# Performance work log

Measured on AMD Instinct MI355X. Metric: run time of the kernel, lower is better.

The kernel has to match this reference:

```python
import jax, jax.numpy as jnp
import numpy as np

N_HEADS = 16
D_EMBED = 1024
D_HEADS = D_EMBED // N_HEADS


def setup_inputs() -> dict:
    key = jax.random.key(0)
    k1, k2, k3, k4, k5 = jax.random.split(key, 5)
    B, S = 4, 2048
    x = jax.random.normal(k1, (B, S, D_EMBED), dtype=jnp.float32)
    s_in = 1.0 / np.sqrt(D_EMBED)
    in_proj_w = jax.random.normal(k2, (3 * D_EMBED, D_EMBED), dtype=jnp.float32) * s_in
    in_proj_b = jax.random.normal(k3, (3 * D_EMBED,), dtype=jnp.float32) * 0.01
    out_proj_w = jax.random.normal(k4, (D_EMBED, D_EMBED), dtype=jnp.float32) * s_in
    out_proj_b = jax.random.normal(k5, (D_EMBED,), dtype=jnp.float32) * 0.01
    return {"x": x, "in_proj_w": in_proj_w, "in_proj_b": in_proj_b,
            "out_proj_w": out_proj_w, "out_proj_b": out_proj_b}


def reference(x, in_proj_w, in_proj_b, out_proj_w, out_proj_b):
    B, S, D = x.shape
    # in_proj: Linear(d, 3d); torch chunks output as (k, q, v) in that order
    qkv = jnp.einsum('bsd,ed->bse', x, in_proj_w) + in_proj_b  # [B,S,3D]
    k, q, v = jnp.split(qkv, 3, axis=-1)
    # reshape to heads: [B, H, S, Dh]
    def to_heads(t):
        return t.reshape(B, S, N_HEADS, D_HEADS).transpose(0, 2, 1, 3)
    q, k, v = to_heads(q), to_heads(k), to_heads(v)
    scale = 1.0 / np.sqrt(D_HEADS)
    w = jnp.einsum('bhqd,bhkd->bhqk', q, k) * scale  # [B,H,S,S]
    w = jax.nn.softmax(w, axis=-1)
    score = jnp.einsum('bhqk,bhkd->bhqd', w, v)  # [B,H,S,Dh]
    score = score.transpose(0, 2, 1, 3).reshape(B, S, D)
    out = jnp.einsum('bsd,ed->bse', score, out_proj_w) + out_proj_b
    return out
```

## Files before the change

kernel.cpp:

```cpp
#include <hip/hip_runtime.h>

typedef __attribute__((ext_vector_type(8))) __bf16 bf16x8;
typedef __attribute__((ext_vector_type(4))) float  f32x4;
typedef __attribute__((ext_vector_type(4))) unsigned short us4;

#define QK_SCALE 0.180336880111112f

__device__ __forceinline__ unsigned short f2bf(float f) {
    unsigned u = __float_as_uint(f);
    u += 0x7fffu + ((u >> 16) & 1u);
    return (unsigned short)(u >> 16);
}

__device__ __forceinline__ unsigned cvt_pk_bf16(float lo, float hi) {
    unsigned r;
    asm("v_cvt_pk_bf16_f32 %0, %1, %2" : "=v"(r) : "v"(lo), "v"(hi));
    return r;
}

__device__ __forceinline__ void gload_lds16(const void* g, void* l) {
    __builtin_amdgcn_global_load_lds((const __attribute__((address_space(1))) void*)g,
                                     (__attribute__((address_space(3))) void*)l, 16, 0, 0);
}

__global__ __launch_bounds__(256) void f32_to_bf16_k(const float* __restrict__ in,
                                                     unsigned short* __restrict__ out, int n) {
    int i = (blockIdx.x * 256 + threadIdx.x) * 4;
    if (i + 3 < n) {
        float4 v = *(const float4*)(in + i);
        us4 o;
        o.x = f2bf(v.x); o.y = f2bf(v.y); o.z = f2bf(v.z); o.w = f2bf(v.w);
        *(us4*)(out + i) = o;
    }
}

__global__ __launch_bounds__(256) void cvt_w1_k(const float* __restrict__ in,
                                                unsigned short* __restrict__ out) {
    int i = (blockIdx.x * 256 + threadIdx.x) * 4;
    float4 v = *(const float4*)(in + i);
    const int row = i >> 10;
    const float s = (row >= 1024 && row < 2048) ? QK_SCALE : 1.0f;
    us4 o;
    o.x = f2bf(v.x * s); o.y = f2bf(v.y * s); o.z = f2bf(v.z * s); o.w = f2bf(v.w * s);
    *(us4*)(out + i) = o;
}

template <int OUTF, int QS>
__global__ __launch_bounds__(256, 2) void gemm_bt(const unsigned short* __restrict__ A,
                                                  const unsigned short* __restrict__ B,
                                                  const float* __restrict__ bias,
                                                  void* __restrict__ Cv,
                                                  int M, int N, int K) {
    __shared__ unsigned short As[4 * 128 * 8];
    __shared__ unsigned short Bs[4 * 128 * 8];
    const int t = threadIdx.x;
    const int lane = t & 63;
    const int w = t >> 6;
    const int wr = w >> 1, wc = w & 1;
    const int lhi = lane >> 4, llo = lane & 15;
    const int bm = blockIdx.y, bn = blockIdx.x;

    f32x4 acc[4][4] = {};

    const unsigned short* Ag = A + (size_t)(bm * 128) * K;
    const unsigned short* Bg = B + (size_t)(bn * 128) * K;

    const int r0 = t & 127, kc0 = t >> 7;
    const int r1 = (256 + t) & 127, kc1 = (256 + t) >> 7;
    const int wbase = (t & ~63) * 8;

    const int KT = K >> 5;
    for (int kt = 0; kt < KT; ++kt) {
        const int k0 = kt * 32;
        gload_lds16(Ag + (size_t)r0 * K + k0 + kc0 * 8, As + wbase);
        gload_lds16(Ag + (size_t)r1 * K + k0 + kc1 * 8, As + 2048 + wbase);
        gload_lds16(Bg + (size_t)r0 * K + k0 + kc0 * 8, Bs + wbase);
        gload_lds16(Bg + (size_t)r1 * K + k0 + kc1 * 8, Bs + 2048 + wbase);
        __syncthreads();

        bf16x8 af[4], bfr[4];
#pragma unroll
        for (int mi = 0; mi < 4; ++mi)
            af[mi] = *(const bf16x8*)(As + lhi * 1024 + (wr * 64 + mi * 16 + llo) * 8);
#pragma unroll
        for (int ni = 0; ni < 4; ++ni)
            bfr[ni] = *(const bf16x8*)(Bs + lhi * 1024 + (wc * 64 + ni * 16 + llo) * 8);
#pragma unroll
        for (int mi = 0; mi < 4; ++mi)
#pragma unroll
            for (int ni = 0; ni < 4; ++ni)
                acc[mi][ni] = __builtin_amdgcn_mfma_f32_16x16x32_bf16(af[mi], bfr[ni], acc[mi][ni], 0, 0, 0);
        __syncthreads();
    }

    const int rowb = bm * 128 + wr * 64;
    const int colb = bn * 128 + wc * 64;
#pragma unroll
    for (int mi = 0; mi < 4; ++mi) {
#pragma unroll
        for (int ni = 0; ni < 4; ++ni) {
            const int col = colb + ni * 16 + llo;
            float bv = bias[col];
            if (QS) bv = (col >= 1024 && col < 2048) ? bv * QK_SCALE : bv;
#pragma unroll
            for (int r = 0; r < 4; ++r) {
                const int row = rowb + mi * 16 + lhi * 4 + r;
                const float v = acc[mi][ni][r] + bv;
                if (OUTF == 0) ((unsigned short*)Cv)[(size_t)row * N + col] = f2bf(v);
                else           ((float*)Cv)[(size_t)row * N + col] = v;
            }
        }
    }
}

__global__ __launch_bounds__(256) void attn_k(const unsigned short* __restrict__ qkv,
                                              unsigned short* __restrict__ score) {
    __shared__ unsigned short Ks[2][4096];
    __shared__ unsigned short Vt[2][5632];

    const int t = threadIdx.x;
    const int lane = t & 63;
    const int w = t >> 6;
    const int lhi = lane >> 4, llo = lane & 15;
    const int b = blockIdx.y >> 4, h = blockIdx.y & 15;
    const int q0 = blockIdx.x * 128;

    const unsigned short* kvb = qkv + (size_t)b * 2048 * 3072 + h * 64;

    bf16x8 qf[2][2];
#pragma unroll
    for (int mf = 0; mf < 2; ++mf) {
        const unsigned short* qp = qkv + (size_t)(b * 2048 + q0 + w * 32 + mf * 16 + llo) * 3072
                                   + 1024 + h * 64 + lhi * 8;
        qf[mf][0] = *(const bf16x8*)qp;
        qf[mf][1] = *(const bf16x8*)(qp + 32);
    }

    f32x4 oacc[2][4] = {};
    float m_[2] = {-1e30f, -1e30f}, l_[2] = {0.f, 0.f};

    const int c = t & 31, vdc = t >> 5;
    const int kA = 4 * ((c >> 2) & 3) + 2 * (c & 1) + 16 * (2 * (c >> 4) + ((c >> 1) & 1));
    const unsigned short* vp = kvb + 2048 + (size_t)kA * 3072 + vdc * 8;
    const unsigned short* kp = kvb + (size_t)lane * 3072 + w * 8;
    bf16x8 vr0, vr1;

    gload_lds16(kp,      &Ks[0][(t & ~63) * 8]);
    gload_lds16(kp + 32, &Ks[0][2048 + (t & ~63) * 8]);
    kp += 196608;
    vr0 = *(const bf16x8*)vp;
    vr1 = *(const bf16x8*)(vp + 3072);
    vp += 196608;

    for (int kt = 0; kt < 32; ++kt) {
        const int cur = kt & 1;
        {
            union { bf16x8 v; unsigned short u[8]; } A_, B_;
            A_.v = vr0; B_.v = vr1;
            unsigned* V32 = (unsigned*)&Vt[cur][0];
#pragma unroll
            for (int j = 0; j < 8; ++j)
                V32[(vdc * 8 + j) * 44 + c] = (unsigned)A_.u[j] | ((unsigned)B_.u[j] << 16);
        }
        __builtin_amdgcn_sched_barrier(0);
        if (kt < 31) {
            vr0 = *(const bf16x8*)vp;
            vr1 = *(const bf16x8*)(vp + 3072);
            vp += 196608;
        }
        __builtin_amdgcn_sched_barrier(0);
        if (kt < 31) asm volatile("s_waitcnt vmcnt(2) lgkmcnt(0)" ::: "memory");
        else         asm volatile("s_waitcnt vmcnt(0) lgkmcnt(0)" ::: "memory");
        __builtin_amdgcn_s_barrier();
        __builtin_amdgcn_sched_barrier(0);
        if (kt < 31) {
            gload_lds16(kp,      &Ks[cur ^ 1][(t & ~63) * 8]);
            gload_lds16(kp + 32, &Ks[cur ^ 1][2048 + (t & ~63) * 8]);
            kp += 196608;
        }

        f32x4 sa[2][4] = {};
#pragma unroll
        for (int ds = 0; ds < 2; ++ds) {
#pragma unroll
            for (int nfk = 0; nfk < 4; ++nfk) {
                bf16x8 kb = *(const bf16x8*)(&Ks[cur][(ds * 4 + lhi) * 512 + (nfk * 16 + llo) * 8]);
                sa[0][nfk] = __builtin_amdgcn_mfma_f32_16x16x32_bf16(kb, qf[0][ds], sa[0][nfk], 0, 0, 0);
                sa[1][nfk] = __builtin_amdgcn_mfma_f32_16x16x32_bf16(kb, qf[1][ds], sa[1][nfk], 0, 0, 0);
            }
        }

        float pmv[2];
#pragma unroll
        for (int mf = 0; mf < 2; ++mf) {
            float p0 = fmaxf(fmaxf(sa[mf][0][0], sa[mf][0][1]), fmaxf(sa[mf][0][2], sa[mf][0][3]));
            float p1 = fmaxf(fmaxf(sa[mf][1][0], sa[mf][1][1]), fmaxf(sa[mf][1][2], sa[mf][1][3]));
            float p2 = fmaxf(fmaxf(sa[mf][2][0], sa[mf][2][1]), fmaxf(sa[mf][2][2], sa[mf][2][3]));
            float p3 = fmaxf(fmaxf(sa[mf][3][0], sa[mf][3][1]), fmaxf(sa[mf][3][2], sa[mf][3][3]));
            float pm = fmaxf(fmaxf(p0, p1), fmaxf(p2, p3));
            pm = fmaxf(pm, __shfl_xor(pm, 16, 64));
            pm = fmaxf(pm, __shfl_xor(pm, 32, 64));
            pmv[mf] = pm;
        }
        const bool grow = (pmv[0] > m_[0] + 8.f) || (pmv[1] > m_[1] + 8.f);
        if (__any(grow)) {
#pragma unroll
            for (int mf = 0; mf < 2; ++mf) {
                const float mn = fmaxf(m_[mf], pmv[mf]);
                const float cc = __builtin_amdgcn_exp2f(m_[mf] - mn);
                m_[mf] = mn;
                l_[mf] *= cc;
                const float c0 = __shfl(cc, lhi * 4 + 0, 64);
                const float c1 = __shfl(cc, lhi * 4 + 1, 64);
                const float c2 = __shfl(cc, lhi * 4 + 2, 64);
                const float c3 = __shfl(cc, lhi * 4 + 3, 64);
#pragma unroll
                for (int nf = 0; nf < 4; ++nf) {
                    oacc[mf][nf][0] *= c0; oacc[mf][nf][1] *= c1;
                    oacc[mf][nf][2] *= c2; oacc[mf][nf][3] *= c3;
                }
            }
        }

        bf16x8 pa[2][2];
#pragma unroll
        for (int mf = 0; mf < 2; ++mf) {
            float p[4][4], s = 0.f;
#pragma unroll
            for (int nf = 0; nf < 4; ++nf)
#pragma unroll
                for (int r = 0; r < 4; ++r) {
                    p[nf][r] = __builtin_amdgcn_exp2f(sa[mf][nf][r] - m_[mf]);
                    s += p[nf][r];
                }
            l_[mf] += s;
            union { unsigned u[4]; bf16x8 v; } k0, k1;
            k0.u[0] = cvt_pk_bf16(p[0][0], p[0][1]); k0.u[1] = cvt_pk_bf16(p[0][2], p[0][3]);
            k0.u[2] = cvt_pk_bf16(p[1][0], p[1][1]); k0.u[3] = cvt_pk_bf16(p[1][2], p[1][3]);
            k1.u[0] = cvt_pk_bf16(p[2][0], p[2][1]); k1.u[1] = cvt_pk_bf16(p[2][2], p[2][3]);
            k1.u[2] = cvt_pk_bf16(p[3][0], p[3][1]); k1.u[3] = cvt_pk_bf16(p[3][2], p[3][3]);
            pa[mf][0] = k0.v; pa[mf][1] = k1.v;
        }

#pragma unroll
        for (int ks = 0; ks < 2; ++ks)
#pragma unroll
            for (int nf = 0; nf < 4; ++nf) {
                bf16x8 vb = *(const bf16x8*)(&Vt[cur][(nf * 16 + llo) * 88 + ks * 32 + lhi * 8]);
                oacc[0][nf] = __builtin_amdgcn_mfma_f32_16x16x32_bf16(pa[0][ks], vb, oacc[0][nf], 0, 0, 0);
                oacc[1][nf] = __builtin_amdgcn_mfma_f32_16x16x32_bf16(pa[1][ks], vb, oacc[1][nf], 0, 0, 0);
            }
    }

#pragma unroll
    for (int mf = 0; mf < 2; ++mf) {
        float l = l_[mf];
        l += __shfl_xor(l, 16, 64);
        l += __shfl_xor(l, 32, 64);
        const float rl = 1.0f / l;
        const float r0 = __shfl(rl, lhi * 4 + 0, 64);
        const float r1 = __shfl(rl, lhi * 4 + 1, 64);
        const float r2 = __shfl(rl, lhi * 4 + 2, 64);
        const float r3 = __shfl(rl, lhi * 4 + 3, 64);
        const int rowb = b * 2048 + q0 + w * 32 + mf * 16;
#pragma unroll
        for (int nf = 0; nf < 4; ++nf) {
            const int col = h * 64 + nf * 16 + llo;
            score[(size_t)(rowb + lhi * 4 + 0) * 1024 + col] = f2bf(oacc[mf][nf][0] * r0);
            score[(size_t)(rowb + lhi * 4 + 1) * 1024 + col] = f2bf(oacc[mf][nf][1] * r1);
            score[(size_t)(rowb + lhi * 4 + 2) * 1024 + col] = f2bf(oacc[mf][nf][2] * r2);
            score[(size_t)(rowb + lhi * 4 + 3) * 1024 + col] = f2bf(oacc[mf][nf][3] * r3);
        }
    }
}

extern "C" void kernel_launch(void* const* d_in, const int* in_sizes, int n_in,
                              void* d_out, int out_size, void* d_ws, size_t ws_size,
                              hipStream_t stream) {
    const float* x  = (const float*)d_in[0];
    const float* w1 = (const float*)d_in[1];
    const float* b1 = (const float*)d_in[2];
    const float* w2 = (const float*)d_in[3];
    const float* b2 = (const float*)d_in[4];
    float* out = (float*)d_out;

    char* ws = (char*)d_ws;
    unsigned short* qkv   = (unsigned short*)ws;
    unsigned short* xbf   = (unsigned short*)(ws + 50331648);
    unsigned short* w1bf  = (unsigned short*)(ws + 50331648 + 16777216);
    unsigned short* w2bf  = (unsigned short*)(ws + 50331648 + 16777216 + 6291456);
    unsigned short* score = xbf;

    f32_to_bf16_k<<<dim3(8388608 / 1024), dim3(256), 0, stream>>>(x,  xbf,  8388608);
    cvt_w1_k<<<dim3(3145728 / 1024), dim3(256), 0, stream>>>(w1, w1bf);
    f32_to_bf16_k<<<dim3(1048576 / 1024), dim3(256), 0, stream>>>(w2, w2bf, 1048576);

    gemm_bt<0, 1><<<dim3(24, 64), dim3(256), 0, stream>>>(xbf, w1bf, b1, (void*)qkv, 8192, 3072, 1024);
    attn_k<<<dim3(16, 64), dim3(256), 0, stream>>>(qkv, score);
    gemm_bt<1, 0><<<dim3(8, 64), dim3(256), 0, stream>>>(score, w2bf, b2, (void*)out, 8192, 1024, 1024);
}
```

Baseline: 283.5 us.

## Rewrite projection GEMMs with double-buffered LDS, 8 waves and swizzled tile order

Replaces the single-buffered 128x128 GEMM with a 512-thread, 128x256-tile kernel. Global-to-LDS loads for the next K step are staged into a second buffer while MFMAs run on the current one, split into four phases with explicit barriers, waitcnts and setprio. Workgroup IDs are swizzled so neighbouring blocks share tiles in cache. It adds more LDS per block, which may lower occupancy, and the hand-written vmcnt ordering is fragile.

```diff
diff --git a/kernel.cpp b/kernel.cpp
--- a/kernel.cpp
+++ b/kernel.cpp
@@ -22,6 +22,8 @@
     __builtin_amdgcn_global_load_lds((const __attribute__((address_space(1))) void*)g,
                                      (__attribute__((address_space(3))) void*)l, 16, 0, 0);
 }
+
+#define SBAR __builtin_amdgcn_sched_barrier(0)
 
 __global__ __launch_bounds__(256) void f32_to_bf16_k(const float* __restrict__ in,
                                                      unsigned short* __restrict__ out, int n) {
@@ -46,55 +48,108 @@
 }
 
 template <int OUTF, int QS>
-__global__ __launch_bounds__(256, 2) void gemm_bt(const unsigned short* __restrict__ A,
+__global__ __launch_bounds__(512, 2) void gemm_dp(const unsigned short* __restrict__ A,
                                                   const unsigned short* __restrict__ B,
                                                   const float* __restrict__ bias,
                                                   void* __restrict__ Cv,
-                                                  int M, int N, int K) {
-    __shared__ unsigned short As[4 * 128 * 8];
-    __shared__ unsigned short Bs[4 * 128 * 8];
+                                                  int MB, int K, int N) {
+    __shared__ unsigned short Al[2][8192];
+    __shared__ unsigned short Bl[2][16384];
+
     const int t = threadIdx.x;
-    const int lane = t & 63;
-    const int w = t >> 6;
-    const int wr = w >> 1, wc = w & 1;
+    const int w = t >> 6, lane = t & 63;
     const int lhi = lane >> 4, llo = lane & 15;
-    const int bm = blockIdx.y, bn = blockIdx.x;
+    const int wr = w >> 2, wc = w & 3;
+
+    const int nwg = gridDim.x;
+    const int id = blockIdx.x;
+    const int swz = (id & 7) * (nwg >> 3) + (id >> 3);
+    const int bn = swz / MB, bm = swz % MB;
+
+    const unsigned short* Ag = A + (size_t)(bm * 128) * K;
+    const unsigned short* Bg = B + (size_t)(bn * 256) * K;
+
+    const unsigned short* aSrc = Ag + (size_t)(t & 127) * K + (t >> 7) * 8;
+    const unsigned short* bSrc = Bg + (size_t)(t & 255) * K + (t >> 8) * 8;
+    const int wb = w * 512;
+
+    auto stageA = [&](int kt, int buf) {
+        const unsigned short* g = aSrc + kt * 64;
+        gload_lds16(g,      &Al[buf][wb]);
+        gload_lds16(g + 32, &Al[buf][wb + 4096]);
+    };
+    auto stageB0 = [&](int kt, int buf) {
+        const unsigned short* g = bSrc + kt * 64;
+        gload_lds16(g,      &Bl[buf][wb]);
+        gload_lds16(g + 16, &Bl[buf][wb + 4096]);
+    };
+    auto stageB1 = [&](int kt, int buf) {
+        const unsigned short* g = bSrc + kt * 64 + 32;
+        gload_lds16(g,      &Bl[buf][wb + 8192]);
+        gload_lds16(g + 16, &Bl[buf][wb + 12288]);
+    };
 
     f32x4 acc[4][4] = {};
-
-    const unsigned short* Ag = A + (size_t)(bm * 128) * K;
-    const unsigned short* Bg = B + (size_t)(bn * 128) * K;
-
-    const int r0 = t & 127, kc0 = t >> 7;
-    const int r1 = (256 + t) & 127, kc1 = (256 + t) >> 7;
-    const int wbase = (t & ~63) * 8;
-
-    const int KT = K >> 5;
+    bf16x8 a[4], bA[2], bB[2];
+
+    auto loadA = [&](int buf, int ds) {
+#pragma unroll
+        for (int mi = 0; mi < 4; ++mi)
+            a[mi] = *(const bf16x8*)(&Al[buf][(ds * 4 + lhi) * 1024 + (wr * 64 + mi * 16 + llo) * 8]);
+    };
+    auto loadB2 = [&](bf16x8* b, int buf, int ds, int nh) {
+#pragma unroll
+        for (int j = 0; j < 2; ++j)
+            b[j] = *(const bf16x8*)(&Bl[buf][(ds * 4 + lhi) * 2048 + (wc * 64 + (nh * 2 + j) * 16 + llo) * 8]);
+    };
+
+#define MFMA8(BV, NB) do {                                                        \
+        _Pragma("unroll")                                                         \
+        for (int mi = 0; mi < 4; ++mi) {                                          \
+            acc[mi][NB]     = __builtin_amdgcn_mfma_f32_16x16x32_bf16(a[mi], BV[0], acc[mi][NB], 0, 0, 0);     \
+            acc[mi][NB + 1] = __builtin_amdgcn_mfma_f32_16x16x32_bf16(a[mi], BV[1], acc[mi][NB + 1], 0, 0, 0); \
+        }                                                                         \
+    } while (0)
+
+    const int KT = K >> 6;
+    stageA(0, 0); stageB0(0, 0); stageB1(0, 0);
+    asm volatile("s_waitcnt vmcnt(2)" ::: "memory");
+    __builtin_amdgcn_s_barrier();
+
     for (int kt = 0; kt < KT; ++kt) {
-        const int k0 = kt * 32;
-        gload_lds16(Ag + (size_t)r0 * K + k0 + kc0 * 8, As + wbase);
-        gload_lds16(Ag + (size_t)r1 * K + k0 + kc1 * 8, As + 2048 + wbase);
-        gload_lds16(Bg + (size_t)r0 * K + k0 + kc0 * 8, Bs + wbase);
-        gload_lds16(Bg + (size_t)r1 * K + k0 + kc1 * 8, Bs + 2048 + wbase);
-        __syncthreads();
-
-        bf16x8 af[4], bfr[4];
-#pragma unroll
-        for (int mi = 0; mi < 4; ++mi)
-            af[mi] = *(const bf16x8*)(As + lhi * 1024 + (wr * 64 + mi * 16 + llo) * 8);
-#pragma unroll
-        for (int ni = 0; ni < 4; ++ni)
-            bfr[ni] = *(const bf16x8*)(Bs + lhi * 1024 + (wc * 64 + ni * 16 + llo) * 8);
-#pragma unroll
-        for (int mi = 0; mi < 4; ++mi)
-#pragma unroll
-            for (int ni = 0; ni < 4; ++ni)
-                acc[mi][ni] = __builtin_amdgcn_mfma_f32_16x16x32_bf16(af[mi], bfr[ni], acc[mi][ni], 0, 0, 0);
-        __syncthreads();
-    }
+        const int cur = kt & 1, nxt = cur ^ 1;
+        const int kn = (kt + 1) & (KT - 1);
+
+        loadA(cur, 0); loadB2(bA, cur, 0, 0);
+        stageA(kn, nxt);
+        SBAR; __builtin_amdgcn_s_barrier(); SBAR;
+        __builtin_amdgcn_s_setprio(1); MFMA8(bA, 0); __builtin_amdgcn_s_setprio(0);
+        SBAR; __builtin_amdgcn_s_barrier();
+
+        loadB2(bB, cur, 0, 1);
+        stageB0(kn, nxt);
+        SBAR; __builtin_amdgcn_s_barrier(); SBAR;
+        __builtin_amdgcn_s_setprio(1); MFMA8(bB, 2); __builtin_amdgcn_s_setprio(0);
+        asm volatile("s_waitcnt vmcnt(4)" ::: "memory");
+        SBAR; __builtin_amdgcn_s_barrier();
+
+        loadA(cur, 1); loadB2(bA, cur, 1, 0);
+        stageB1(kn, nxt);
+        SBAR; __builtin_amdgcn_s_barrier(); SBAR;
+        __builtin_amdgcn_s_setprio(1); MFMA8(bA, 0); __builtin_amdgcn_s_setprio(0);
+        SBAR; __builtin_amdgcn_s_barrier();
+
+        loadB2(bB, cur, 1, 1);
+        SBAR; __builtin_amdgcn_s_barrier(); SBAR;
+        __builtin_amdgcn_s_setprio(1); MFMA8(bB, 2); __builtin_amdgcn_s_setprio(0);
+        asm volatile("s_waitcnt vmcnt(2)" ::: "memory");
+        SBAR; __builtin_amdgcn_s_barrier();
+    }
+    asm volatile("s_waitcnt vmcnt(0)" ::: "memory");
+#undef MFMA8
 
     const int rowb = bm * 128 + wr * 64;
-    const int colb = bn * 128 + wc * 64;
+    const int colb = bn * 256 + wc * 64;
 #pragma unroll
     for (int mi = 0; mi < 4; ++mi) {
 #pragma unroll
@@ -295,7 +350,7 @@
     cvt_w1_k<<<dim3(3145728 / 1024), dim3(256), 0, stream>>>(w1, w1bf);
     f32_to_bf16_k<<<dim3(1048576 / 1024), dim3(256), 0, stream>>>(w2, w2bf, 1048576);
 
-    gemm_bt<0, 1><<<dim3(24, 64), dim3(256), 0, stream>>>(xbf, w1bf, b1, (void*)qkv, 8192, 3072, 1024);
+    gemm_dp<0, 1><<<dim3(768), dim3(512), 0, stream>>>(xbf, w1bf, b1, (void*)qkv, 64, 1024, 3072);
     attn_k<<<dim3(16, 64), dim3(256), 0, stream>>>(qkv, score);
-    gemm_bt<1, 0><<<dim3(8, 64), dim3(256), 0, stream>>>(score, w2bf, b2, (void*)out, 8192, 1024, 1024);
-}
+    gemm_dp<1, 0><<<dim3(256), dim3(512), 0, stream>>>(score, w2bf, b2, (void*)out, 64, 1024, 1024);
+}
```

Measured after the change: 304.4 us. +7.3%, slower.

## Double-buffer GEMM LDS tiles and fuse conversion kernels into one launch

Applied to the files above, without the earlier changes.

The projection GEMM now keeps two LDS buffers and issues global-to-LDS loads for the next K tile before computing the current one. It waits with a partial vmcnt so load latency overlaps the MFMA work. Separately, the three fp32-to-bf16 conversion kernels are merged into one launch to cut launch overhead. Doubling the LDS buffers could reduce occupancy, and the manual waitcnt depends on the exact number of loads outstanding.

```diff
diff --git a/kernel.cpp b/kernel.cpp
--- a/kernel.cpp
+++ b/kernel.cpp
@@ -5,6 +5,7 @@
 typedef __attribute__((ext_vector_type(4))) unsigned short us4;
 
 #define QK_SCALE 0.180336880111112f
+#define SBAR __builtin_amdgcn_sched_barrier(0)
 
 __device__ __forceinline__ unsigned short f2bf(float f) {
     unsigned u = __float_as_uint(f);
@@ -23,26 +24,30 @@
                                      (__attribute__((address_space(3))) void*)l, 16, 0, 0);
 }
 
-__global__ __launch_bounds__(256) void f32_to_bf16_k(const float* __restrict__ in,
-                                                     unsigned short* __restrict__ out, int n) {
-    int i = (blockIdx.x * 256 + threadIdx.x) * 4;
-    if (i + 3 < n) {
-        float4 v = *(const float4*)(in + i);
-        us4 o;
-        o.x = f2bf(v.x); o.y = f2bf(v.y); o.z = f2bf(v.z); o.w = f2bf(v.w);
-        *(us4*)(out + i) = o;
-    }
-}
-
-__global__ __launch_bounds__(256) void cvt_w1_k(const float* __restrict__ in,
-                                                unsigned short* __restrict__ out) {
-    int i = (blockIdx.x * 256 + threadIdx.x) * 4;
-    float4 v = *(const float4*)(in + i);
-    const int row = i >> 10;
-    const float s = (row >= 1024 && row < 2048) ? QK_SCALE : 1.0f;
+__global__ __launch_bounds__(256) void cvt_all_k(const float* __restrict__ x,
+                                                 const float* __restrict__ w1,
+                                                 const float* __restrict__ w2,
+                                                 unsigned short* __restrict__ xbf,
+                                                 unsigned short* __restrict__ w1bf,
+                                                 unsigned short* __restrict__ w2bf) {
+    const int i = (blockIdx.x * 256 + threadIdx.x) * 4;
+    const float* src;
+    unsigned short* dst;
+    int li;
+    float s = 1.0f;
+    if (i < 8388608) {
+        src = x; dst = xbf; li = i;
+    } else if (i < 11534336) {
+        li = i - 8388608; src = w1; dst = w1bf;
+        const int row = li >> 10;
+        if (row >= 1024 && row < 2048) s = QK_SCALE;
+    } else {
+        li = i - 11534336; src = w2; dst = w2bf;
+    }
+    float4 v = *(const float4*)(src + li);
     us4 o;
     o.x = f2bf(v.x * s); o.y = f2bf(v.y * s); o.z = f2bf(v.z * s); o.w = f2bf(v.w * s);
-    *(us4*)(out + i) = o;
+    *(us4*)(dst + li) = o;
 }
 
 template <int OUTF, int QS>
@@ -51,8 +56,8 @@
                                                   const float* __restrict__ bias,
                                                   void* __restrict__ Cv,
                                                   int M, int N, int K) {
-    __shared__ unsigned short As[4 * 128 * 8];
-    __shared__ unsigned short Bs[4 * 128 * 8];
+    __shared__ unsigned short As[2][4096];
+    __shared__ unsigned short Bs[2][4096];
     const int t = threadIdx.x;
     const int lane = t & 63;
     const int w = t >> 6;
@@ -69,28 +74,40 @@
     const int r1 = (256 + t) & 127, kc1 = (256 + t) >> 7;
     const int wbase = (t & ~63) * 8;
 
+    auto stage = [&](int kt, int buf) {
+        const int k0 = kt * 32;
+        gload_lds16(Ag + (size_t)r0 * K + k0 + kc0 * 8, &As[buf][wbase]);
+        gload_lds16(Ag + (size_t)r1 * K + k0 + kc1 * 8, &As[buf][2048 + wbase]);
+        gload_lds16(Bg + (size_t)r0 * K + k0 + kc0 * 8, &Bs[buf][wbase]);
+        gload_lds16(Bg + (size_t)r1 * K + k0 + kc1 * 8, &Bs[buf][2048 + wbase]);
+    };
+
     const int KT = K >> 5;
+    stage(0, 0);
     for (int kt = 0; kt < KT; ++kt) {
-        const int k0 = kt * 32;
-        gload_lds16(Ag + (size_t)r0 * K + k0 + kc0 * 8, As + wbase);
-        gload_lds16(Ag + (size_t)r1 * K + k0 + kc1 * 8, As + 2048 + wbase);
-        gload_lds16(Bg + (size_t)r0 * K + k0 + kc0 * 8, Bs + wbase);
-        gload_lds16(Bg + (size_t)r1 * K + k0 + kc1 * 8, Bs + 2048 + wbase);
-        __syncthreads();
+        const int cur = kt & 1;
+        if (kt < KT - 1) stage(kt + 1, cur ^ 1);
+        SBAR;
+        if (kt < KT - 1) asm volatile("s_waitcnt vmcnt(4)" ::: "memory");
+        else             asm volatile("s_waitcnt vmcnt(0)" ::: "memory");
+        __builtin_amdgcn_s_barrier();
+        SBAR;
 
         bf16x8 af[4], bfr[4];
 #pragma unroll
         for (int mi = 0; mi < 4; ++mi)
-            af[mi] = *(const bf16x8*)(As + lhi * 1024 + (wr * 64 + mi * 16 + llo) * 8);
+            af[mi] = *(const bf16x8*)(&As[cur][lhi * 1024 + (wr * 64 + mi * 16 + llo) * 8]);
 #pragma unroll
         for (int ni = 0; ni < 4; ++ni)
-            bfr[ni] = *(const bf16x8*)(Bs + lhi * 1024 + (wc * 64 + ni * 16 + llo) * 8);
+            bfr[ni] = *(const bf16x8*)(&Bs[cur][lhi * 1024 + (wc * 64 + ni * 16 + llo) * 8]);
 #pragma unroll
         for (int mi = 0; mi < 4; ++mi)
 #pragma unroll
             for (int ni = 0; ni < 4; ++ni)
                 acc[mi][ni] = __builtin_amdgcn_mfma_f32_16x16x32_bf16(af[mi], bfr[ni], acc[mi][ni], 0, 0, 0);
-        __syncthreads();
+        SBAR;
+        __builtin_amdgcn_s_barrier();
+        SBAR;
     }
 
     const int rowb = bm * 128 + wr * 64;
@@ -291,9 +308,7 @@
     unsigned short* w2bf  = (unsigned short*)(ws + 50331648 + 16777216 + 6291456);
     unsigned short* score = xbf;
 
-    f32_to_bf16_k<<<dim3(8388608 / 1024), dim3(256), 0, stream>>>(x,  xbf,  8388608);
-    cvt_w1_k<<<dim3(3145728 / 1024), dim3(256), 0, stream>>>(w1, w1bf);
-    f32_to_bf16_k<<<dim3(1048576 / 1024), dim3(256), 0, stream>>>(w2, w2bf, 1048576);
+    cvt_all_k<<<dim3(12288), dim3(256), 0, stream>>>(x, w1, w2, xbf, w1bf, w2bf);
 
     gemm_bt<0, 1><<<dim3(24, 64), dim3(256), 0, stream>>>(xbf, w1bf, b1, (void*)qkv, 8192, 3072, 1024);
     attn_k<<<dim3(16, 64), dim3(256), 0, stream>>>(qkv, score);
```

Result: no change. 281.4 us (-0.7%).
